# Optimization experiments

Measured on AMD Instinct MI355X. Metric: run time of the kernel, lower is better.

Reference implementation:

```python
import jax, jax.numpy as jnp
import numpy as np
from jax import lax

B, A, H, W = 4, 9, 128, 128
FEAT_STRIDE = 16
PRE_NMS_TOPN = 4000
POST_NMS_TOPN = 1000
NMS_THRESH = 0.7
IM_SIZE = 2048.0


def _generate_anchors(base_size=16, ratios=(0.5, 1.0, 2.0), scales=(8.0, 16.0, 32.0)):
    base = np.array([1.0, 1.0, base_size, base_size], dtype=np.float32) - 1.0

    def whctrs(a):
        w = a[2] - a[0] + 1.0
        h = a[3] - a[1] + 1.0
        return w, h, a[0] + 0.5 * (w - 1.0), a[1] + 0.5 * (h - 1.0)

    def mk(ws, hs, xc, yc):
        ws = ws[:, None]
        hs = hs[:, None]
        return np.hstack([xc - 0.5 * (ws - 1.0), yc - 0.5 * (hs - 1.0),
                          xc + 0.5 * (ws - 1.0), yc + 0.5 * (hs - 1.0)])

    w, h, xc, yc = whctrs(base)
    size = w * h
    r = np.array(ratios, dtype=np.float32)
    ws = np.round(np.sqrt(size / r))
    hs = np.round(ws * r)
    ratio_anchors = mk(ws, hs, xc, yc)
    out = []
    s = np.array(scales, dtype=np.float32)
    for a in ratio_anchors:
        w2, h2, xc2, yc2 = whctrs(a)
        out.append(mk(w2 * s, h2 * s, xc2, yc2))
    return np.vstack(out).astype(np.float32)  # [A, 4]


ANCHORS = jnp.asarray(_generate_anchors(FEAT_STRIDE))


def setup_inputs() -> dict:
    key = jax.random.key(0)
    k1, k2 = jax.random.split(key)
    scores = jax.random.normal(k1, (B, 2 * A, H, W), dtype=jnp.float32)
    bbox_deltas = jax.random.normal(k2, (B, 4 * A, H, W), dtype=jnp.float32) * 0.5
    im_info = jnp.tile(jnp.array([IM_SIZE, IM_SIZE, 1.0], dtype=jnp.float32), (B, 1))
    valid_range = jnp.tile(jnp.array([0.0, 10000.0], dtype=jnp.float32), (B, 1))
    return {"scores": scores, "bbox_deltas": bbox_deltas, "im_info": im_info,
            "valid_range": valid_range}


def _bbox_transform_inv(anchors, deltas):
    # anchors [N,4] broadcast against deltas [B,N,4]
    w = anchors[..., 2] - anchors[..., 0] + 1.0
    h = anchors[..., 3] - anchors[..., 1] + 1.0
    cx = anchors[..., 0] + 0.5 * w
    cy = anchors[..., 1] + 0.5 * h
    dx, dy, dw, dh = deltas[..., 0], deltas[..., 1], deltas[..., 2], deltas[..., 3]
    pcx = dx * w + cx
    pcy = dy * h + cy
    pw = jnp.exp(dw) * w
    ph = jnp.exp(dh) * h
    return jnp.stack([pcx - 0.5 * pw, pcy - 0.5 * ph,
                      pcx + 0.5 * pw, pcy + 0.5 * ph], axis=-1)


def _clip_boxes(boxes, im_hw):
    # boxes [B,N,4]; im_hw [B,2] = (height, width)
    boxes = jnp.maximum(boxes, 0.0)
    hmax = im_hw[:, 0][:, None] - 1.0
    wmax = im_hw[:, 1][:, None] - 1.0
    return jnp.stack([jnp.minimum(boxes[..., 0], wmax),
                      jnp.minimum(boxes[..., 1], hmax),
                      jnp.minimum(boxes[..., 2], wmax),
                      jnp.minimum(boxes[..., 3], hmax)], axis=-1)


def _iou_matrix(boxes):
    # boxes [N,4], +1 pixel convention (matches gpu_nms)
    x1, y1, x2, y2 = boxes[:, 0], boxes[:, 1], boxes[:, 2], boxes[:, 3]
    areas = (x2 - x1 + 1.0) * (y2 - y1 + 1.0)
    iw = jnp.maximum(jnp.minimum(x2[:, None], x2[None, :]) - jnp.maximum(x1[:, None], x1[None, :]) + 1.0, 0.0)
    ih = jnp.maximum(jnp.minimum(y2[:, None], y2[None, :]) - jnp.maximum(y1[:, None], y1[None, :]) + 1.0, 0.0)
    inter = iw * ih
    return inter / (areas[:, None] + areas[None, :] - inter)


def _nms_single(proposals, scores_flat):
    # proposals [KA,4], scores_flat [KA] -> [POST,4] zero-padded, score-ordered
    _, order = lax.top_k(scores_flat, PRE_NMS_TOPN)
    boxes = proposals[order]  # [PRE,4] sorted by descending score
    sup_mat = lax.stop_gradient(_iou_matrix(boxes) > NMS_THRESH)
    idxs = jnp.arange(PRE_NMS_TOPN)

    def body(i, supp):
        row = sup_mat[i] & (idxs > i)
        return jnp.where(supp[i], supp, supp | row)

    supp = lax.fori_loop(0, PRE_NMS_TOPN, body, jnp.zeros(PRE_NMS_TOPN, dtype=bool))
    keep = ~supp
    # stable argsort puts kept indices first, preserving score order
    kidx = jnp.argsort(jnp.where(keep, 0, 1), stable=True)[:POST_NMS_TOPN]
    valid = (jnp.arange(POST_NMS_TOPN) < keep.sum()).astype(boxes.dtype)
    return boxes[kidx] * valid[:, None]


def reference(scores, bbox_deltas, im_info, valid_range):
    fg = scores[:, A:, :, :]                      # [B,A,Hf,Wf] objectness scores
    Bc, _, Hf, Wf = fg.shape
    # anchor grid: [K,4] shifts + [A,4] base anchors -> [K*A,4]
    sx = jnp.arange(Wf, dtype=jnp.float32) * FEAT_STRIDE
    sy = jnp.arange(Hf, dtype=jnp.float32) * FEAT_STRIDE
    gx, gy = jnp.meshgrid(sx, sy)                 # [Hf,Wf] (xy indexing like np.meshgrid)
    shifts = jnp.stack([gx.ravel(), gy.ravel(), gx.ravel(), gy.ravel()], axis=1)  # [K,4]
    anchors = (ANCHORS[None, :, :] + shifts[:, None, :]).reshape(-1, 4)           # [K*A,4]

    deltas = bbox_deltas.transpose(0, 2, 3, 1).reshape(Bc, -1, 4)  # [B,K*A,4]
    sc = fg.transpose(0, 2, 3, 1).reshape(Bc, -1)                   # [B,K*A]

    proposals = _bbox_transform_inv(anchors[None, :, :], deltas)
    proposals = _clip_boxes(proposals, im_info[:, :2])

    # filter_proposal_by_range: area = w*h (no +1), score -> -1 if out of range
    widths = proposals[..., 2] - proposals[..., 0]
    heights = proposals[..., 3] - proposals[..., 1]
    area = widths * heights
    min_a = (valid_range[:, 0] ** 2)[:, None]
    max_a = (valid_range[:, 1] ** 2)[:, None]
    sc = jnp.where((area < min_a) | (area > max_a), -1.0, sc)

    out_boxes = jax.vmap(_nms_single)(proposals, sc)  # [B,POST,4]
    batch_col = jnp.broadcast_to(
        jnp.arange(Bc, dtype=out_boxes.dtype)[:, None, None], (Bc, POST_NMS_TOPN, 1))
    return jnp.concatenate([batch_col, out_boxes], axis=-1)  # [B,POST,5]
```

## Files before the change

### kernel.cpp

```cpp
#include <hip/hip_runtime.h>
#include <cmath>

#define WD 128
#define HT 128
#define HW 16384
#define NB 4
#define NA 9
#define NPB (NA*HW)
#define TOPN 4000
#define POSTN 1000
#define CANDCAP 8192
#define REPCAP 1024
#define NREPL 32
#define MROWS 4096
#define RST 4160
#define NTILE 63
#define TRI (NTILE*(NTILE+1)/2)
#define NREP 4
#define NBINS 4096
#define NBLK 42

typedef unsigned long long u64;
typedef unsigned int u32;

struct Anchors { float v[36]; };

static void gen_anchors(float* out) {
    double base[4] = {0.0, 0.0, 15.0, 15.0};
    const double ratios[3] = {0.5, 1.0, 2.0};
    const double scales[3] = {8.0, 16.0, 32.0};
    double w = base[2] - base[0] + 1.0;
    double h = base[3] - base[1] + 1.0;
    double xc = base[0] + 0.5 * (w - 1.0);
    double yc = base[1] + 0.5 * (h - 1.0);
    double size = w * h;
    double ra[3][4];
    for (int r = 0; r < 3; ++r) {
        double ws = nearbyint(sqrt(size / ratios[r]));
        double hs = nearbyint(ws * ratios[r]);
        ra[r][0] = xc - 0.5 * (ws - 1.0);
        ra[r][1] = yc - 0.5 * (hs - 1.0);
        ra[r][2] = xc + 0.5 * (ws - 1.0);
        ra[r][3] = yc + 0.5 * (hs - 1.0);
    }
    int k = 0;
    for (int r = 0; r < 3; ++r) {
        double w2 = ra[r][2] - ra[r][0] + 1.0;
        double h2 = ra[r][3] - ra[r][1] + 1.0;
        double x2c = ra[r][0] + 0.5 * (w2 - 1.0);
        double y2c = ra[r][1] + 0.5 * (h2 - 1.0);
        for (int s = 0; s < 3; ++s) {
            double ws = w2 * scales[s], hs = h2 * scales[s];
            out[k*4+0] = (float)(x2c - 0.5 * (ws - 1.0));
            out[k*4+1] = (float)(y2c - 0.5 * (hs - 1.0));
            out[k*4+2] = (float)(x2c + 0.5 * (ws - 1.0));
            out[k*4+3] = (float)(y2c + 0.5 * (hs - 1.0));
            ++k;
        }
    }
}

__device__ __forceinline__ u32 sortable_key(float sc) {
    u32 sb = __float_as_uint(sc);
    return sb ^ ((sb & 0x80000000u) ? 0xFFFFFFFFu : 0x80000000u);
}

__device__ __forceinline__ u64 readlane64(u64 v, int l) {
    u32 lo = (u32)__builtin_amdgcn_readlane((int)(u32)v, l);
    u32 hi = (u32)__builtin_amdgcn_readlane((int)(u32)(v >> 32), l);
    return ((u64)hi << 32) | lo;
}

__device__ __forceinline__ u64 wave_or64_dpp(u64 v) {
    u32 lo = (u32)v, hi = (u32)(v >> 32);
#define DPPOR(x, ctrl) x |= (u32)__builtin_amdgcn_update_dpp(0, (int)(x), ctrl, 0xf, 0xf, false)
    DPPOR(lo, 0x111); DPPOR(lo, 0x112); DPPOR(lo, 0x114); DPPOR(lo, 0x118);
    DPPOR(lo, 0x142); DPPOR(lo, 0x143);
    DPPOR(hi, 0x111); DPPOR(hi, 0x112); DPPOR(hi, 0x114); DPPOR(hi, 0x118);
    DPPOR(hi, 0x142); DPPOR(hi, 0x143);
#undef DPPOR
    u32 rlo = (u32)__builtin_amdgcn_readlane((int)lo, 63);
    u32 rhi = (u32)__builtin_amdgcn_readlane((int)hi, 63);
    return ((u64)rhi << 32) | rlo;
}

__device__ __forceinline__ float4 decode_box(const float* __restrict__ deltas,
                                             const float* __restrict__ im_info,
                                             const Anchors& A, int b, int a, int p)
{
#pragma clang fp contract(off)
    int hh = p >> 7;
    int ww = p & 127;
    float sx = (float)(ww * 16);
    float sy = (float)(hh * 16);
    float ax1 = A.v[a*4+0] + sx;
    float ay1 = A.v[a*4+1] + sy;
    float ax2 = A.v[a*4+2] + sx;
    float ay2 = A.v[a*4+3] + sy;
    const float* dbase = deltas + ((size_t)(b*36 + a*4))*HW + p;
    float dx = dbase[0];
    float dy = dbase[HW];
    float dw = dbase[2*HW];
    float dh = dbase[3*HW];
    float aw = ax2 - ax1 + 1.0f;
    float ah = ay2 - ay1 + 1.0f;
    float cx = ax1 + 0.5f*aw;
    float cy = ay1 + 0.5f*ah;
    float pcx = dx*aw + cx;
    float pcy = dy*ah + cy;
    float ew = (float)exp((double)dw);
    float eh = (float)exp((double)dh);
    float pw = ew * aw;
    float ph = eh * ah;
    float x1 = pcx - 0.5f*pw;
    float y1 = pcy - 0.5f*ph;
    float x2 = pcx + 0.5f*pw;
    float y2 = pcy + 0.5f*ph;
    float hmax = im_info[b*3+0] - 1.0f;
    float wmax = im_info[b*3+1] - 1.0f;
    x1 = fmaxf(x1, 0.0f); y1 = fmaxf(y1, 0.0f);
    x2 = fmaxf(x2, 0.0f); y2 = fmaxf(y2, 0.0f);
    x1 = fminf(x1, wmax); y1 = fminf(y1, hmax);
    x2 = fminf(x2, wmax); y2 = fminf(y2, hmax);
    return make_float4(x1, y1, x2, y2);
}

__global__ void k_props(const float* __restrict__ scores,
                        const float* __restrict__ deltas,
                        const float* __restrict__ im_info,
                        const float* __restrict__ valid_range,
                        Anchors A,
                        u32* __restrict__ fkeys,
                        u32* __restrict__ hist12)
{
#pragma clang fp contract(off)
    __shared__ u32 lh[NBINS];
    int tid = threadIdx.x;
#pragma unroll
    for (int i = 0; i < NBINS/256; ++i) lh[tid + i*256] = 0;
    __syncthreads();

    int n = blockIdx.x * 256 + tid;
    int b = n / NPB;
    int r = n - b*NPB;
    int a = r / HW;
    int p = r - a*HW;

    float4 bx = decode_box(deltas, im_info, A, b, a, p);
    float sc = scores[((size_t)(b*18 + 9 + a))*HW + p];
    float area = (bx.z - bx.x) * (bx.w - bx.y);
    float v0 = valid_range[b*2+0], v1 = valid_range[b*2+1];
    if (area < v0*v0 || area > v1*v1) sc = -1.0f;

    u32 key = sortable_key(sc);
    fkeys[n] = key;
    atomicAdd(&lh[key >> 20], 1u);
    __syncthreads();

    int rep = blockIdx.x & (NREP-1);
    u32* gh = hist12 + ((size_t)rep*NB + b)*NBINS;
#pragma unroll
    for (int i = 0; i < NBINS/256; ++i) {
        u32 v = lh[tid + i*256];
        if (v) atomicAdd(&gh[tid + i*256], v);
    }
}

__global__ void k_findT(const u32* __restrict__ hist12, u32* __restrict__ thresh12)
{
    __shared__ u32 sfx[1024];
    int b = blockIdx.x, t = threadIdx.x;
    u32 bin0 = 0, bin1 = 0, bin2 = 0, bin3 = 0;
    for (int rr = 0; rr < NREP; ++rr) {
        const u32* h = hist12 + ((size_t)rr*NB + b)*NBINS + t*4;
        bin0 += h[0]; bin1 += h[1]; bin2 += h[2]; bin3 += h[3];
    }
    u32 s4 = bin0 + bin1 + bin2 + bin3;
    sfx[t] = s4;
    __syncthreads();
    for (int d = 1; d < 1024; d <<= 1) {
        u32 add = (t + d < 1024) ? sfx[t + d] : 0u;
        __syncthreads();
        sfx[t] += add;
        __syncthreads();
    }
    u32 above = (t < 1023) ? sfx[t+1] : 0u;
    u32 c3 = bin3 + above;
    u32 c2 = bin2 + c3;
    u32 c1 = bin1 + c2;
    u32 c0 = bin0 + c1;
    if (c3 >= TOPN && above < TOPN) thresh12[b] = (u32)(t*4 + 3);
    if (c2 >= TOPN && c3    < TOPN) thresh12[b] = (u32)(t*4 + 2);
    if (c1 >= TOPN && c2    < TOPN) thresh12[b] = (u32)(t*4 + 1);
    if (c0 >= TOPN && c1    < TOPN) thresh12[b] = (u32)(t*4 + 0);
}

__global__ void k_emit(const u32* __restrict__ fkeys,
                       const u32* __restrict__ thresh12,
                       u32* __restrict__ ccntRep,
                       u64* __restrict__ cand)
{
    int tid = threadIdx.x;
    int n = blockIdx.x * 256 + tid;
    int b = n / NPB;
    int r = n - b*NPB;
    int a = r / HW;
    int p = r - a*HW;
    u32 key = fkeys[n];
    bool cond = (key >> 20) >= thresh12[b];
    u64 m = __ballot(cond);
    int lane = tid & 63;
    int rep = blockIdx.x & (NREPL-1);
    if (cond) {
        int leader = __ffsll((unsigned long long)m) - 1;
        u32 base = 0;
        if (lane == leader)
            base = atomicAdd(&ccntRep[(b*NREPL + rep)*16], (u32)__popcll(m));
        base = (u32)__shfl((int)base, leader);
        u32 pos = base + (u32)__popcll(m & ((1ull << lane) - 1ull));
        if (pos < REPCAP) {
            u32 t = (u32)(p*NA + a);
            cand[((size_t)b*NREPL + rep)*REPCAP + pos] = ((u64)key << 32) | (u32)(~t);
        }
    }
}

__global__ void k_rank2(const u64* __restrict__ cand, const u32* __restrict__ ccntRep,
                        const float* __restrict__ deltas,
                        const float* __restrict__ im_info,
                        Anchors A,
                        float4* __restrict__ topk)
{
    __shared__ u64 kk[CANDCAP];
    __shared__ u32 ps[256];
    __shared__ u32 rcnt[32];
    __shared__ u32 roff[33];
    int b = blockIdx.y;
    int tid = threadIdx.x;
    if (tid < 32) {
        u32 c = ccntRep[(b*NREPL + tid)*16];
        rcnt[tid] = (c > REPCAP) ? REPCAP : c;
    }
    __syncthreads();
    if (tid == 0) {
        u32 acc = 0;
        for (int i = 0; i < 32; ++i) { roff[i] = acc; acc += rcnt[i]; }
        roff[32] = (acc > CANDCAP) ? CANDCAP : acc;
    }
    __syncthreads();
    u32 N = roff[32];
    if ((u32)(blockIdx.x * 64) >= N) return;
    for (int rr = 0; rr < 32; ++rr) {
        u32 len = rcnt[rr], base = roff[rr];
        const u64* src = cand + ((size_t)b*NREPL + rr)*REPCAP;
        for (u32 i = tid; i < len; i += 256) {
            u32 g = base + i;
            if (g < CANDCAP) kk[g] = src[i];
        }
    }
    __syncthreads();
    int kl = tid & 63, seg = tid >> 6;
    u32 ki = (u32)(blockIdx.x * 64 + kl);
    u64 mykey = (ki < N) ? kk[ki] : ~0ull;
    u32 segN = (N + 3) >> 2;
    u32 s0 = seg * segN;
    u32 s1 = s0 + segN; if (s1 > N) s1 = N;
    u32 pr = 0;
    u32 i = s0;
    for (; i + 16 <= s1; i += 16) {
        u64 v0 = kk[i+0],  v1 = kk[i+1],  v2 = kk[i+2],  v3 = kk[i+3];
        u64 v4 = kk[i+4],  v5 = kk[i+5],  v6 = kk[i+6],  v7 = kk[i+7];
        u64 v8 = kk[i+8],  v9 = kk[i+9],  va = kk[i+10], vb = kk[i+11];
        u64 vc = kk[i+12], vd = kk[i+13], ve = kk[i+14], vf = kk[i+15];
        pr += (v0 > mykey) + (v1 > mykey) + (v2 > mykey) + (v3 > mykey);
        pr += (v4 > mykey) + (v5 > mykey) + (v6 > mykey) + (v7 > mykey);
        pr += (v8 > mykey) + (v9 > mykey) + (va > mykey) + (vb > mykey);
        pr += (vc > mykey) + (vd > mykey) + (ve > mykey) + (vf > mykey);
    }
    for (; i < s1; ++i) pr += (kk[i] > mykey) ? 1u : 0u;
    ps[tid] = pr;
    __syncthreads();
    if (seg == 0 && ki < N) {
        u32 rank = ps[kl] + ps[kl+64] + ps[kl+128] + ps[kl+192];
        if (rank < TOPN) {
            u32 t = ~((u32)mykey);
            int a = (int)(t % 9u);
            int p = (int)(t / 9u);
            topk[(size_t)b*MROWS + rank] = decode_box(deltas, im_info, A, b, a, p);
        }
    }
}

__global__ void k_mask(const float4* __restrict__ topk, u64* __restrict__ masksT)
{
#pragma clang fp contract(off)
    int L = blockIdx.x;
    int b = blockIdx.y;
    int ti = (int)((2.0*NTILE + 1.0 -
                    sqrt((2.0*NTILE + 1.0)*(2.0*NTILE + 1.0) - 8.0*(double)L)) * 0.5);
    while ((ti+1)*NTILE - ((ti+1)*ti)/2 <= L) ++ti;
    while (ti*NTILE - (ti*(ti-1))/2 > L) --ti;
    int tj = ti + (L - (ti*NTILE - (ti*(ti-1))/2));

    int r = threadIdx.x;
    int i = ti*64 + r;
    __shared__ float4 cb[64];
    __shared__ float  ca[64];
    u64 word = 0;
    {
        int jj = tj*64 + r;
        float4 cbox = (jj < TOPN) ? topk[(size_t)b*MROWS + jj] : make_float4(0,0,0,0);
        cb[r] = cbox;
        ca[r] = (cbox.z - cbox.x + 1.0f) * (cbox.w - cbox.y + 1.0f);
        __syncthreads();
        if (i < TOPN) {
            float4 rb = topk[(size_t)b*MROWS + i];
            float rarea = (rb.z - rb.x + 1.0f) * (rb.w - rb.y + 1.0f);
            for (int q = 0; q < 64; ++q) {
                float4 cc = cb[q];
                float iw = fminf(rb.z, cc.z) - fmaxf(rb.x, cc.x) + 1.0f;
                float ih = fminf(rb.w, cc.w) - fmaxf(rb.y, cc.y) + 1.0f;
                iw = fmaxf(iw, 0.0f); ih = fmaxf(ih, 0.0f);
                float inter = iw * ih;
                float uni = (rarea + ca[q]) - inter;
                float iou = inter / uni;
                if (iou > 0.7f) word |= (1ULL << q);
            }
            int nvalid = TOPN - tj*64;
            if (nvalid < 64) word &= ((1ULL << nvalid) - 1ULL);
            if (ti == tj) {
                u64 cm = (r == 63) ? ~0ULL : ((1ULL << (r + 1)) - 1ULL);
                word &= ~cm;
            }
        }
    }
    masksT[((size_t)(b*64 + tj))*RST + i] = word;
}

#define NMS_PLOAD(cc) { \
    int cm = ((cc) > 62) ? 62 : (cc); \
    const u64* colp = mb + (size_t)cm*RST; \
    _Pragma("unroll") \
    for (int k = 0; k < NBLK; ++k) \
        if (k <= cm) pf[k] = colp[(size_t)k*64 + lane]; \
}

#define NMS_PSTORE(cc, BUF) { \
    int cm = ((cc) > 62) ? 62 : (cc); \
    int wmax = (cm < NBLK-1) ? cm+1 : NBLK; \
    _Pragma("unroll") \
    for (int k = 0; k < NBLK; ++k) \
        if (k < wmax) (BUF)[k*64 + lane] = pf[k]; \
}

__global__ __launch_bounds__(128, 1) void k_nms(const u64* __restrict__ masksT,
                      const float4* __restrict__ topk,
                      float* __restrict__ out)
{
    int b = blockIdx.x;
    int tid = threadIdx.x;
    int lane = tid & 63;
    int wid = tid >> 6;

    __shared__ u64 colbuf[2][NBLK*64];
    __shared__ u32 kmexp[64][64];
    __shared__ u64 kmw[64];
    __shared__ u64 wcomm[1];
    __shared__ int exitf;

    if (wid == 0) {
        kmw[lane] = 0ull;
#pragma unroll
        for (int k = 0; k < 32; ++k) kmexp[k][lane] = 0u;
    } else {
#pragma unroll
        for (int k = 32; k < 64; ++k) kmexp[k][lane] = 0u;
    }
    if (tid == 0) { wcomm[0] = 0ull; exitf = 0; }

    const u64* mb = masksT + (size_t)b*64*RST;

    u64 pf[NBLK];
    u64 accp = 0;

    if (wid == 0) {
        float* ob = out + (size_t)b*POSTN*5;
        for (int e = lane; e < POSTN*5; e += 64)
            ob[e] = ((e % 5) == 0) ? (float)b : 0.0f;
    } else {
        NMS_PLOAD(0)
        NMS_PSTORE(0, colbuf[0])
        NMS_PLOAD(1)
    }

    int kcnt = 0;
    for (int c = 0; c < 63; ++c) {
        int cur = c & 1;
        __syncthreads();
        if (exitf) break;
        if (wid == 1) {
            u64 acc = accp;
            if (c > 0) {
                u32 mk = kmexp[c-1][lane];
                u64 v = (c-1 < NBLK) ? colbuf[cur][(c-1)*64 + lane]
                                     : mb[(size_t)c*RST + (size_t)(c-1)*64 + lane];
                acc |= v & (((u64)mk << 32) | mk);
                for (int k = NBLK; k < c-1; ++k) {
                    u32 m2 = kmexp[k][lane];
                    u64 v2 = mb[(size_t)c*RST + (size_t)k*64 + lane];
                    acc |= v2 & (((u64)m2 << 32) | m2);
                }
            }
            u64 wv = wave_or64_dpp(acc);
            if (lane == 0) wcomm[0] = wv;
        }
        __syncthreads();
        if (wid == 0) {
            u64 wl = wcomm[0];
            u32 wlo = (u32)__builtin_amdgcn_readfirstlane((int)(u32)wl);
            u32 whi = (u32)__builtin_amdgcn_readfirstlane((int)(u32)(wl >> 32));
            u64 w = ((u64)whi << 32) | wlo;
            u64 D = (c < NBLK) ? colbuf[cur][c*64 + lane]
                               : mb[(size_t)c*RST + (size_t)c*64 + lane];
#pragma unroll
            for (int g = 0; g < 4; ++g) {
                u64 drs[16];
#pragma unroll
                for (int j = 0; j < 16; ++j) drs[j] = readlane64(D, g*16 + j);
#pragma unroll
                for (int j = 0; j < 16; ++j) {
                    u64 t;
                    asm("s_bitcmp1_b64 %[w], %[rr]\n\t"
                        "s_cselect_b64 %[t], 0, %[d]\n\t"
                        "s_or_b64 %[w], %[w], %[t]"
                        : [w]"+s"(w), [t]"=&s"(t)
                        : [d]"s"(drs[j]), [rr]"i"(g*16 + j)
                        : "scc");
                }
            }
            u64 kmask = ~w & ((c < 62) ? ~0ull : 0xFFFFFFFFull);
            kcnt += __popcll(kmask);
            if (lane == 0) {
                kmw[c] = kmask;
                if (kcnt >= POSTN || c == 62) exitf = 1;
            }
            kmexp[c][lane] = ((u32)((kmask >> lane) & 1ull)) ? ~0u : 0u;
        } else {
            NMS_PSTORE(c+1, colbuf[cur^1])
            u64 ap = 0;
            int km = (c < NBLK) ? c : NBLK;
#pragma unroll
            for (int k = 0; k < NBLK; ++k) {
                if (k < km) {
                    u32 mk = kmexp[k][lane];
                    ap |= pf[k] & (((u64)mk << 32) | mk);
                }
            }
            accp = ap;
            NMS_PLOAD(c+2)
        }
    }

    if (wid == 0) {
        u64 keepw = kmw[lane];
        int cnt = __popcll(keepw);
        int pre = cnt;
        for (int d = 1; d < 64; d <<= 1) {
            int t = __shfl_up(pre, d);
            if (lane >= d) pre += t;
        }
        int excl = pre - cnt;
        asm volatile("s_waitcnt vmcnt(0)" ::: "memory");
        u64 wv = keepw; int rk = excl;
        while (wv) {
            int bpos = __ffsll((unsigned long long)wv) - 1;
            wv &= wv - 1;
            if (rk < POSTN) {
                int i = lane*64 + bpos;
                float4 bx = topk[(size_t)b*MROWS + i];
                float* o = out + ((size_t)b*POSTN + rk)*5;
                o[1] = bx.x; o[2] = bx.y; o[3] = bx.z; o[4] = bx.w;
            }
            ++rk;
        }
    }
}

extern "C" void kernel_launch(void* const* d_in, const int* in_sizes, int n_in,
                              void* d_out, int out_size, void* d_ws, size_t ws_size,
                              hipStream_t stream)
{
    const float* scores  = (const float*)d_in[0];
    const float* deltas  = (const float*)d_in[1];
    const float* im_info = (const float*)d_in[2];
    const float* vrange  = (const float*)d_in[3];
    float* out = (float*)d_out;

    char* ws = (char*)d_ws;
    size_t off = 0;
    auto alloc = [&](size_t bytes) -> void* {
        void* ptr = ws + off;
        off += (bytes + 255) & ~(size_t)255;
        return ptr;
    };
    u32*   fkeys   = (u32*)   alloc((size_t)NB*NPB*sizeof(u32));
    u64*   cand    = (u64*)   alloc((size_t)NB*NREPL*REPCAP*sizeof(u64));
    float4* topk   = (float4*)alloc((size_t)NB*MROWS*sizeof(float4));
    u64*   masksT  = (u64*)   alloc((size_t)NB*64*RST*sizeof(u64));
    u32*   hist12  = (u32*)   alloc((size_t)NREP*NB*NBINS*sizeof(u32));
    u32*   ccntRep = (u32*)   alloc((size_t)NB*NREPL*16*sizeof(u32));
    u32*   thresh12= (u32*)   alloc(256);

    Anchors A;
    gen_anchors(A.v);

    size_t zbytes = (char*)ccntRep + (size_t)NB*NREPL*16*sizeof(u32) - (char*)hist12;
    hipMemsetAsync(hist12, 0, zbytes, stream);

    int total = NB*NPB;
    int blocks = (total + 255)/256;
    k_props<<<blocks, 256, 0, stream>>>(scores, deltas, im_info, vrange, A, fkeys, hist12);
    k_findT<<<NB, 1024, 0, stream>>>(hist12, thresh12);
    k_emit<<<blocks, 256, 0, stream>>>(fkeys, thresh12, ccntRep, cand);
    dim3 rgrid(CANDCAP/64, NB);
    k_rank2<<<rgrid, 256, 0, stream>>>(cand, ccntRep, deltas, im_info, A, topk);
    dim3 mgrid(TRI, NB);
    k_mask<<<mgrid, 64, 0, stream>>>(topk, masksT);
    k_nms<<<NB, 128, 0, stream>>>(masksT, topk, out);
}
```

Before: 124.0 us.

## Split NMS suppression accumulation across two extra waves and drop a barrier

The NMS kernel grows from two to four waves. One wave now only streams mask columns into the shared double buffer. Two waves each OR-accumulate half of the earlier kept-block masks and publish partial words to shared memory one iteration ahead. The serial wave folds in the previous block's contribution itself, which removes the second __syncthreads per column step and shortens the per-iteration critical path. The cost is more registers per wave and more LDS traffic, and correctness relies on the one-step-ahead partial timing.

```diff
diff --git a/kernel.cpp b/kernel.cpp
--- a/kernel.cpp
+++ b/kernel.cpp
@@ -19,6 +19,7 @@
 #define NREP 4
 #define NBINS 4096
 #define NBLK 42
+#define HBLK 21
 
 typedef unsigned long long u64;
 typedef unsigned int u32;
@@ -353,7 +354,15 @@
         if (k < wmax) (BUF)[k*64 + lane] = pf[k]; \
 }
 
-__global__ __launch_bounds__(128, 1) void k_nms(const u64* __restrict__ masksT,
+#define NMS_PLOAD2(cc, H0) { \
+    int cm = ((cc) > 62) ? 62 : (cc); \
+    const u64* colp = mb + (size_t)cm*RST; \
+    _Pragma("unroll") \
+    for (int k = 0; k < HBLK; ++k) \
+        if ((H0) + k <= cm) pf2[k] = colp[(size_t)((H0) + k)*64 + lane]; \
+}
+
+__global__ __launch_bounds__(256, 1) void k_nms(const u64* __restrict__ masksT,
                       const float4* __restrict__ topk,
                       float* __restrict__ out)
 {
@@ -365,61 +374,58 @@
     __shared__ u64 colbuf[2][NBLK*64];
     __shared__ u32 kmexp[64][64];
     __shared__ u64 kmw[64];
-    __shared__ u64 wcomm[1];
+    __shared__ u64 wpart[2][2];
     __shared__ int exitf;
 
     if (wid == 0) {
         kmw[lane] = 0ull;
 #pragma unroll
-        for (int k = 0; k < 32; ++k) kmexp[k][lane] = 0u;
+        for (int k = 0; k < 16; ++k) kmexp[k][lane] = 0u;
     } else {
 #pragma unroll
-        for (int k = 32; k < 64; ++k) kmexp[k][lane] = 0u;
-    }
-    if (tid == 0) { wcomm[0] = 0ull; exitf = 0; }
+        for (int k = 0; k < 16; ++k) kmexp[wid*16 + k][lane] = 0u;
+    }
+    if (tid == 0) {
+        wpart[0][0] = 0ull; wpart[0][1] = 0ull;
+        wpart[1][0] = 0ull; wpart[1][1] = 0ull;
+        exitf = 0;
+    }
 
     const u64* mb = masksT + (size_t)b*64*RST;
 
     u64 pf[NBLK];
-    u64 accp = 0;
+    u64 pf2[HBLK];
+    int h0 = (wid == 3) ? HBLK : 0;
 
     if (wid == 0) {
         float* ob = out + (size_t)b*POSTN*5;
         for (int e = lane; e < POSTN*5; e += 64)
             ob[e] = ((e % 5) == 0) ? (float)b : 0.0f;
-    } else {
+    } else if (wid == 1) {
         NMS_PLOAD(0)
         NMS_PSTORE(0, colbuf[0])
         NMS_PLOAD(1)
-    }
-
+    } else {
+        NMS_PLOAD2(1, h0)
+    }
+
+    u64 kmask_prev = 0ull;
     int kcnt = 0;
     for (int c = 0; c < 63; ++c) {
         int cur = c & 1;
         __syncthreads();
         if (exitf) break;
-        if (wid == 1) {
-            u64 acc = accp;
+        if (wid == 0) {
+            u64 wv0 = wpart[cur][0] | wpart[cur][1];
             if (c > 0) {
-                u32 mk = kmexp[c-1][lane];
-                u64 v = (c-1 < NBLK) ? colbuf[cur][(c-1)*64 + lane]
-                                     : mb[(size_t)c*RST + (size_t)(c-1)*64 + lane];
-                acc |= v & (((u64)mk << 32) | mk);
-                for (int k = NBLK; k < c-1; ++k) {
-                    u32 m2 = kmexp[k][lane];
-                    u64 v2 = mb[(size_t)c*RST + (size_t)k*64 + lane];
-                    acc |= v2 & (((u64)m2 << 32) | m2);
-                }
-            }
-            u64 wv = wave_or64_dpp(acc);
-            if (lane == 0) wcomm[0] = wv;
-        }
-        __syncthreads();
-        if (wid == 0) {
-            u64 wl = wcomm[0];
-            u32 wlo = (u32)__builtin_amdgcn_readfirstlane((int)(u32)wl);
-            u32 whi = (u32)__builtin_amdgcn_readfirstlane((int)(u32)(wl >> 32));
-            u64 w = ((u64)whi << 32) | wlo;
+                u64 ltD = (c-1 < NBLK) ? colbuf[cur][(c-1)*64 + lane]
+                                       : mb[(size_t)c*RST + (size_t)(c-1)*64 + lane];
+                u64 sel = ((kmask_prev >> lane) & 1ull) ? ltD : 0ull;
+                wv0 |= wave_or64_dpp(sel);
+            }
+            u32 wlo_ = (u32)__builtin_amdgcn_readfirstlane((int)(u32)wv0);
+            u32 whi_ = (u32)__builtin_amdgcn_readfirstlane((int)(u32)(wv0 >> 32));
+            u64 w = ((u64)whi_ << 32) | wlo_;
             u64 D = (c < NBLK) ? colbuf[cur][c*64 + lane]
                                : mb[(size_t)c*RST + (size_t)c*64 + lane];
 #pragma unroll
@@ -445,19 +451,31 @@
                 if (kcnt >= POSTN || c == 62) exitf = 1;
             }
             kmexp[c][lane] = ((u32)((kmask >> lane) & 1ull)) ? ~0u : 0u;
+            kmask_prev = kmask;
+        } else if (wid == 1) {
+            NMS_PSTORE(c+1, colbuf[cur^1])
+            NMS_PLOAD(c+2)
         } else {
-            NMS_PSTORE(c+1, colbuf[cur^1])
             u64 ap = 0;
             int km = (c < NBLK) ? c : NBLK;
 #pragma unroll
-            for (int k = 0; k < NBLK; ++k) {
-                if (k < km) {
+            for (int k = 0; k < HBLK; ++k) {
+                if (h0 + k < km) {
+                    u32 mk = kmexp[h0 + k][lane];
+                    ap |= pf2[k] & (((u64)mk << 32) | mk);
+                }
+            }
+            if (wid == 3) {
+                int ccl = (c+1 > 62) ? 62 : (c+1);
+                for (int k = NBLK; k < c; ++k) {
                     u32 mk = kmexp[k][lane];
-                    ap |= pf[k] & (((u64)mk << 32) | mk);
+                    u64 v2 = mb[(size_t)ccl*RST + (size_t)k*64 + lane];
+                    ap |= v2 & (((u64)mk << 32) | mk);
                 }
             }
-            accp = ap;
-            NMS_PLOAD(c+2)
+            u64 wr = wave_or64_dpp(ap);
+            if (lane == 0) wpart[cur^1][wid-2] = wr;
+            NMS_PLOAD2(c+2, h0)
         }
     }
 
@@ -515,7 +533,7 @@
     gen_anchors(A.v);
 
     size_t zbytes = (char*)ccntRep + (size_t)NB*NREPL*16*sizeof(u32) - (char*)hist12;
-    hipMemsetAsync(hist12, 0, zbytes, stream);
+    (void)hipMemsetAsync(hist12, 0, zbytes, stream);
 
     int total = NB*NPB;
     int blocks = (total + 255)/256;
@@ -526,5 +544,5 @@
     k_rank2<<<rgrid, 256, 0, stream>>>(cand, ccntRep, deltas, im_info, A, topk);
     dim3 mgrid(TRI, NB);
     k_mask<<<mgrid, 64, 0, stream>>>(topk, masksT);
-    k_nms<<<NB, 128, 0, stream>>>(masksT, topk, out);
-}
+    k_nms<<<NB, 256, 0, stream>>>(masksT, topk, out);
+}
```

Result: faster. 121.5 us (-2.0%).
